# Kernel optimization log

Hardware: AMD Instinct MI355X
Metric: run time of the kernel (lower is better)

## Reference

```python
import jax, jax.numpy as jnp
import numpy as np

QK = 64
KNN = 16
EPS = 1e-5


def conv1(x, w, b):
    # x: (B,C,N), w: (O,C) -> (B,O,N)
    return jnp.einsum('oc,bcn->bon', w, x) + b[None, :, None]


def conv2(x, w, b):
    # x: (B,C,N,k), w: (O,C) -> (B,O,N,k)
    return jnp.einsum('oc,bcnk->bonk', w, x) + b[None, :, None, None]


def bn1(x, g, b, m, v):
    return g[None, :, None] * (x - m[None, :, None]) * jax.lax.rsqrt(v + EPS)[None, :, None] + b[None, :, None]


def bn2(x, g, b, m, v):
    return g[None, :, None, None] * (x - m[None, :, None, None]) * jax.lax.rsqrt(v + EPS)[None, :, None, None] + b[None, :, None, None]


def gather_nk(t, idx):
    # t: (B,C,M), idx: (B,N,k) -> (B,C,N,k)
    return jax.vmap(lambda tb, ib: tb[:, ib])(t, idx)


def setup_inputs():
    key = jax.random.key(0)
    ks = jax.random.split(key, 40)
    B, N, M = 2, 16384, 4096
    w = lambda k, s: jax.random.normal(k, s, dtype=jnp.float32) * 0.05
    d = {}
    d['xyz_hr'] = jax.random.normal(ks[0], (B, 3, N), dtype=jnp.float32)
    d['xyz_lr'] = jax.random.normal(ks[1], (B, 3, M), dtype=jnp.float32)
    d['sft_feat_lr'] = jax.random.normal(ks[2], (B, 6, M), dtype=jnp.float32)
    d['val_lr'] = jax.random.normal(ks[3], (B, 64, M), dtype=jnp.float32)
    # geom_encoder: Conv1d(3,64) -> BN -> ReLU -> Conv1d(64,64)
    d['ge_w1'] = w(ks[4], (QK, 3)); d['ge_b1'] = w(ks[5], (QK,))
    d['ge_g1'] = jnp.ones((QK,)); d['ge_be1'] = jnp.zeros((QK,))
    d['ge_m1'] = w(ks[6], (QK,)); d['ge_v1'] = jax.random.uniform(ks[7], (QK,), minval=0.5, maxval=1.5)
    d['ge_w2'] = w(ks[8], (QK, QK)); d['ge_b2'] = w(ks[9], (QK,))
    # scale/shift convs Conv1d(6,64)
    d['sc_w'] = w(ks[10], (QK, 6)); d['sc_b'] = w(ks[11], (QK,))
    d['sh_w'] = w(ks[12], (QK, 6)); d['sh_b'] = w(ks[13], (QK,))
    # sem query/key Conv1d(64,64)
    d['q_w'] = w(ks[14], (QK, QK)); d['q_b'] = w(ks[15], (QK,))
    d['k_w'] = w(ks[16], (QK, QK)); d['k_b'] = w(ks[17], (QK,))
    # bdy_head: Conv1d(64,64) -> BN -> ReLU -> Conv1d(64,1) -> Sigmoid
    d['bd_w1'] = w(ks[18], (64, QK)); d['bd_b1'] = w(ks[19], (64,))
    d['bd_g'] = jnp.ones((64,)); d['bd_be'] = jnp.zeros((64,))
    d['bd_m'] = w(ks[20], (64,)); d['bd_v'] = jax.random.uniform(ks[21], (64,), minval=0.5, maxval=1.5)
    d['bd_w2'] = w(ks[22], (1, 64)); d['bd_b2'] = w(ks[23], (1,))
    # rel_pos_mlp: Conv2d(3,64) -> BN2d -> ReLU -> Conv2d(64,64)
    d['rp_w1'] = w(ks[24], (QK, 3)); d['rp_b1'] = w(ks[25], (QK,))
    d['rp_g'] = jnp.ones((QK,)); d['rp_be'] = jnp.zeros((QK,))
    d['rp_m'] = w(ks[26], (QK,)); d['rp_v'] = jax.random.uniform(ks[27], (QK,), minval=0.5, maxval=1.5)
    d['rp_w2'] = w(ks[28], (QK, QK)); d['rp_b2'] = w(ks[29], (QK,))
    return d


def reference(xyz_hr, xyz_lr, sft_feat_lr, val_lr,
              ge_w1, ge_b1, ge_g1, ge_be1, ge_m1, ge_v1, ge_w2, ge_b2,
              sc_w, sc_b, sh_w, sh_b, q_w, q_b, k_w, k_b,
              bd_w1, bd_b1, bd_g, bd_be, bd_m, bd_v, bd_w2, bd_b2,
              rp_w1, rp_b1, rp_g, rp_be, rp_m, rp_v, rp_w2, rp_b2):
    B, _, M = sft_feat_lr.shape
    curr_k = min(KNN, M)

    def geom_enc(x):
        h = jax.nn.relu(bn1(conv1(x, ge_w1, ge_b1), ge_g1, ge_be1, ge_m1, ge_v1))
        return conv1(h, ge_w2, ge_b2)

    geom_hr = geom_enc(xyz_hr)                     # (B,64,N)
    geom_lr = geom_enc(xyz_lr)                     # (B,64,M)
    scale = conv1(sft_feat_lr, sc_w, sc_b)
    shift = conv1(sft_feat_lr, sh_w, sh_b)
    geom_lr_mod = geom_lr * (scale + 1.0) + shift
    Q = conv1(geom_hr, q_w, q_b)                   # (B,64,N)
    K = conv1(geom_lr_mod, k_w, k_b)               # (B,64,M)
    # boundary head
    h = jax.nn.relu(bn1(conv1(geom_hr, bd_w1, bd_b1), bd_g, bd_be, bd_m, bd_v))
    bdy_prob = jax.nn.sigmoid(conv1(h, bd_w2, bd_b2))  # (B,1,N)
    # kNN via squared distances (same argmin ordering as torch.cdist)
    hr_t = jnp.swapaxes(xyz_hr, 1, 2)              # (B,N,3)
    lr_t = jnp.swapaxes(xyz_lr, 1, 2)              # (B,M,3)
    d2 = (jnp.sum(hr_t**2, -1)[:, :, None] + jnp.sum(lr_t**2, -1)[:, None, :]
          - 2.0 * jnp.einsum('bnd,bmd->bnm', hr_t, lr_t))  # (B,N,M)
    _, k_idx = jax.lax.top_k(-d2, curr_k)          # (B,N,k) int32
    k_idx = jax.lax.stop_gradient(k_idx)

    K_g = gather_nk(K, k_idx)                      # (B,64,N,k)
    xyz_lr_g = gather_nk(xyz_lr, k_idx)            # (B,3,N,k)
    rel_pos = xyz_hr[:, :, :, None] - xyz_lr_g     # (B,3,N,k)
    pe = jax.nn.relu(bn2(conv2(rel_pos, rp_w1, rp_b1), rp_g, rp_be, rp_m, rp_v))
    pos_enc = conv2(pe, rp_w2, rp_b2)              # (B,64,N,k)
    logits = jnp.sum(Q[:, :, :, None] * (K_g + pos_enc), axis=1) / np.sqrt(QK)  # (B,N,k)
    attn = jax.nn.softmax(logits, axis=-1)
    val_g = gather_nk(val_lr, k_idx)               # (B,Cv,N,k)
    out = jnp.sum(attn[:, None, :, :] * val_g, axis=-1)  # (B,Cv,N)
    return out, bdy_prob
```

## Files before the change

### kernel.cpp

```cpp
#include <hip/hip_runtime.h>
#include <hip/hip_bf16.h>

#define B_ 2
#define N_ 16384
#define M_ 4096
#define EPS_ 1e-5f

typedef float f32x2 __attribute__((ext_vector_type(2)));
typedef float f32x4 __attribute__((ext_vector_type(4)));

__device__ __forceinline__ float b2f(const __hip_bfloat16 v) { return __bfloat162float(v); }

__device__ __forceinline__ float ldin(const void* p, size_t i, int f32) {
    return f32 ? ((const float*)p)[i] : __bfloat162float(((const __hip_bfloat16*)p)[i]);
}
__device__ __forceinline__ void stout(void* o, size_t i, float v, int f32) {
    if (f32) ((float*)o)[i] = v;
    else     ((__hip_bfloat16*)o)[i] = __float2bfloat16(v);
}

__device__ __forceinline__ float d2np(float x, float y, float z, float hn, float4 q) {
    float dot = __fadd_rn(__fadd_rn(__fmul_rn(x, q.x), __fmul_rn(y, q.y)), __fmul_rn(z, q.z));
    return __fsub_rn(__fadd_rn(hn, q.w), __fmul_rn(2.f, dot));
}
__device__ __forceinline__ float norm3np(float x, float y, float z) {
    return __fadd_rn(__fadd_rn(__fmul_rn(x, x), __fmul_rn(y, y)), __fmul_rn(z, z));
}

#define O_GE_W1 0
#define O_GE_B1 192
#define O_GE_W2 256
#define O_GE_B2 4352
#define O_QW    4416
#define O_QB    8512
#define O_KW    8576
#define O_KB    12672
#define O_SCW   12736
#define O_SCB   13120
#define O_SHW   13184
#define O_SHB   13568
#define O_BDW1  13632
#define O_BDB1  17728
#define O_BDW2  17792
#define O_BDB2  17856
#define O_RPW1  17920
#define O_RPB1  18112
#define O_RPW2  18176
#define O_RPB2  22272
#define OB_LR    92160
#define OB_Q     223232
#define OB_KT    4417536
#define OB_VT    5466112
#define OB_KIDX  6514688
#define OB_DFLAG 7694336
#define OB_PA1   7563264
#define OB_PA2   7628800
#define O_T_GE_W2 1923840
#define O_T_QW    1927936
#define O_T_KW    1932032
#define O_T_BDW1  1936128

#define TMAX 256

__global__ __launch_bounds__(256) void prep_kernel(
    const void* xyz_hr,
    const void* ge_w1, const void* ge_b1, const void* ge_g1, const void* ge_be1,
    const void* ge_m1, const void* ge_v1, const void* ge_w2, const void* ge_b2,
    const void* sc_w, const void* sc_b, const void* sh_w, const void* sh_b,
    const void* q_w, const void* q_b, const void* k_w, const void* k_b,
    const void* bd_w1, const void* bd_b1, const void* bd_g, const void* bd_be,
    const void* bd_m, const void* bd_v, const void* bd_w2, const void* bd_b2,
    const void* rp_w1, const void* rp_b1, const void* rp_g, const void* rp_be,
    const void* rp_m, const void* rp_v, const void* rp_w2, const void* rp_b2,
    float* W, int* dflag)
{
    __shared__ int scnt;
    int t = threadIdx.x;
    if (t == 0) scnt = 0;
    __syncthreads();
    if (t < 128) {
        unsigned short u = ((const unsigned short*)xyz_hr)[t];
        int e = (u >> 7) & 0xFF;
        int ok = (e >= 113 && e <= 132) || ((u & 0x7FFF) == 0);
        if (ok) atomicAdd(&scnt, 1);
    }
    __syncthreads();
    const int f32 = (scnt < 110) ? 1 : 0;
    if (t == 0) *dflag = f32;

    if (t < 64) {
        float s = ldin(ge_g1, t, f32) * rsqrtf(ldin(ge_v1, t, f32) + EPS_);
        for (int d = 0; d < 3; ++d) W[O_GE_W1 + t*3 + d] = s * ldin(ge_w1, t*3 + d, f32);
        W[O_GE_B1 + t] = s * (ldin(ge_b1, t, f32) - ldin(ge_m1, t, f32)) + ldin(ge_be1, t, f32);
        W[O_GE_B2 + t] = ldin(ge_b2, t, f32);
        W[O_QB + t] = ldin(q_b, t, f32);
        W[O_KB + t] = ldin(k_b, t, f32);
        W[O_SCB + t] = ldin(sc_b, t, f32);
        W[O_SHB + t] = ldin(sh_b, t, f32);
        float sb = ldin(bd_g, t, f32) * rsqrtf(ldin(bd_v, t, f32) + EPS_);
        W[O_BDB1 + t] = sb * (ldin(bd_b1, t, f32) - ldin(bd_m, t, f32)) + ldin(bd_be, t, f32);
        W[O_BDW2 + t] = ldin(bd_w2, t, f32);
        float sr = ldin(rp_g, t, f32) * rsqrtf(ldin(rp_v, t, f32) + EPS_);
        for (int d = 0; d < 3; ++d) W[O_RPW1 + t*3 + d] = sr * ldin(rp_w1, t*3 + d, f32);
        W[O_RPB1 + t] = sr * (ldin(rp_b1, t, f32) - ldin(rp_m, t, f32)) + ldin(rp_be, t, f32);
        W[O_RPB2 + t] = ldin(rp_b2, t, f32);
    }
    if (t == 0) W[O_BDB2] = ldin(bd_b2, 0, f32);
    for (int i = t; i < 4096; i += 256) {
        int c = i >> 6, r = i & 63;
        float w2 = ldin(ge_w2, i, f32);
        float qw = ldin(q_w, i, f32);
        float kw = ldin(k_w, i, f32);
        float sb = ldin(bd_g, c, f32) * rsqrtf(ldin(bd_v, c, f32) + EPS_);
        float bw = sb * ldin(bd_w1, i, f32);
        W[O_GE_W2 + i] = w2;
        W[O_QW + i]    = qw;
        W[O_KW + i]    = kw;
        W[O_RPW2 + i]  = ldin(rp_w2, i, f32);
        W[O_BDW1 + i]  = bw;
        W[O_T_GE_W2 + r*64 + c] = w2;
        W[O_T_QW    + r*64 + c] = qw;
        W[O_T_KW    + r*64 + c] = kw;
        W[O_T_BDW1  + r*64 + c] = bw;
    }
    for (int i = t; i < 384; i += 256) {
        W[O_SCW + i] = ldin(sc_w, i, f32);
        W[O_SHW + i] = ldin(sh_w, i, f32);
    }
}

__global__ __launch_bounds__(256) void lr_kernel(
    const void* __restrict__ xyz_lr,
    const void* __restrict__ sft,
    const void* __restrict__ val,
    const float* __restrict__ W,
    __hip_bfloat16* __restrict__ Kt, __hip_bfloat16* __restrict__ Vt,
    float4* __restrict__ LR, float* __restrict__ PA1, float* __restrict__ PA2,
    const int* dflag)
{
    const int f32 = *dflag;
    int lane = threadIdx.x & 63;
    int p = blockIdx.x * 4 + (threadIdx.x >> 6);
    int b = p >> 12, m = p & (M_ - 1);
    size_t base = (size_t)b*3*M_ + m;
    float x = ldin(xyz_lr, base, f32), y = ldin(xyz_lr, base + M_, f32), z = ldin(xyz_lr, base + 2*M_, f32);
    if (lane == 0) {
        float hn = norm3np(x, y, z);
        LR[p] = make_float4(x, y, z, hn);
        int k = m >> 1, o = m & 1;
        float* a1 = PA1 + ((size_t)b*2048 + k)*4;
        float* a2 = PA2 + ((size_t)b*2048 + k)*4;
        a1[o] = x; a1[2+o] = y;
        a2[o] = z; a2[2+o] = hn;
    }

    const float* w1 = W + O_GE_W1 + lane*3;
    float h = fmaxf(fmaf(w1[2], z, fmaf(w1[1], y, fmaf(w1[0], x, W[O_GE_B1 + lane]))), 0.f);
    float g = W[O_GE_B2 + lane];
#pragma unroll
    for (int i = 0; i < 64; ++i) {
        g = fmaf(W[O_T_GE_W2 + i*64 + lane], __shfl(h, i, 64), g);
    }
    float sc = W[O_SCB + lane], sh = W[O_SHB + lane];
    const float* wsc = W + O_SCW + lane*6;
    const float* wsh = W + O_SHW + lane*6;
#pragma unroll
    for (int d = 0; d < 6; ++d) {
        float s6 = ldin(sft, (size_t)b*6*M_ + d*M_ + m, f32);
        sc = fmaf(wsc[d], s6, sc); sh = fmaf(wsh[d], s6, sh);
    }
    float mod = fmaf(g, sc + 1.f, sh);
    float k = W[O_KB + lane];
#pragma unroll
    for (int i = 0; i < 64; ++i) {
        k = fmaf(W[O_T_KW + i*64 + lane], __shfl(mod, i, 64), k);
    }
    Kt[(size_t)p*64 + lane] = __float2bfloat16(k);
    Vt[(size_t)p*64 + lane] = __float2bfloat16(ldin(val, (size_t)b*64*M_ + (size_t)lane*M_ + m, f32));
}

__global__ __launch_bounds__(256) void hr_kernel(
    const void* __restrict__ xyz_hr,
    const float* __restrict__ W,
    __hip_bfloat16* __restrict__ Q,
    void* __restrict__ out, const int* dflag)
{
    const int f32 = *dflag;
    int lane = threadIdx.x & 63;
    int p = blockIdx.x * 4 + (threadIdx.x >> 6);
    int b = p >> 14, n = p & (N_ - 1);
    size_t base = (size_t)b*3*N_ + n;
    float x = ldin(xyz_hr, base, f32), y = ldin(xyz_hr, base + N_, f32), z = ldin(xyz_hr, base + 2*N_, f32);

    const float* w1 = W + O_GE_W1 + lane*3;
    float h = fmaxf(fmaf(w1[2], z, fmaf(w1[1], y, fmaf(w1[0], x, W[O_GE_B1 + lane]))), 0.f);
    float g = W[O_GE_B2 + lane];
#pragma unroll
    for (int i = 0; i < 64; ++i) {
        g = fmaf(W[O_T_GE_W2 + i*64 + lane], __shfl(h, i, 64), g);
    }
    float q = W[O_QB + lane];
#pragma unroll
    for (int i = 0; i < 64; ++i) {
        q = fmaf(W[O_T_QW + i*64 + lane], __shfl(g, i, 64), q);
    }
    Q[(size_t)p*64 + lane] = __float2bfloat16(q);
    float hb = W[O_BDB1 + lane];
#pragma unroll
    for (int i = 0; i < 64; ++i) {
        hb = fmaf(W[O_T_BDW1 + i*64 + lane], __shfl(g, i, 64), hb);
    }
    float o = W[O_BDW2 + lane] * fmaxf(hb, 0.f);
#pragma unroll
    for (int sh = 1; sh < 64; sh <<= 1) o += __shfl_xor(o, sh, 64);
    if (lane == 0) {
        o += W[O_BDB2];
        stout(out, (size_t)B_*64*N_ + (size_t)b*N_ + n, 1.f / (1.f + __expf(-o)), f32);
    }
}

#define CE(da, ia, db, ib) { \
    bool sw_ = (db < da) || (db == da && ib < ia); \
    float td_ = da; int ti_ = ia; \
    da = sw_ ? db : da; ia = sw_ ? ib : ia; \
    db = sw_ ? td_ : db; ib = sw_ ? ti_ : ib; }

__device__ __forceinline__ void topk_insert(float (&bd)[16], int (&bi)[16], float d2, int m) {
    if (d2 < bd[15] || (d2 == bd[15] && m < bi[15])) {
        bd[15] = d2; bi[15] = m;
#pragma unroll
        for (int j = 15; j > 0; --j) CE(bd[j-1], bi[j-1], bd[j], bi[j]);
    }
}

__device__ __forceinline__ int lesslex(uint2 e, float cd, int ci) {
    float dj = __uint_as_float(e.x);
    int   ij = (int)e.y;
    return (dj < cd || (dj == cd && ij < ci)) ? 1 : 0;
}

__global__ __launch_bounds__(256, 4) void knn_kernel(
    const void* __restrict__ xyz_hr,
    const float4* __restrict__ LR,
    const f32x4* __restrict__ PA1, const f32x4* __restrict__ PA2,
    unsigned short* __restrict__ kidx, const int* dflag)
{
#pragma clang fp reassociate(off)
#pragma clang fp contract(off)
    __shared__ uint2 scand[4 * TMAX];
    const int f32 = *dflag;
    int lane = threadIdx.x & 63;
    int wid  = threadIdx.x >> 6;
    int p = blockIdx.x * 4 + wid;
    int b = p >> 14, n = p & (N_ - 1);
    size_t base = (size_t)b*3*N_ + n;
    float x = ldin(xyz_hr, base, f32), y = ldin(xyz_hr, base + N_, f32), z = ldin(xyz_hr, base + 2*N_, f32);
    float hn = norm3np(x, y, z);
    const float4* L = LR + b*M_;
    const f32x4* P1 = PA1 + (size_t)b*2048;
    const f32x4* P2 = PA2 + (size_t)b*2048;

    f32x2 d2p[32];
    float v = 3.4e38f;
    f32x2 xx = {x, x}, yy = {y, y}, zz = {z, z}, hh = {hn, hn};
#pragma unroll
    for (int c = 0; c < 8; ++c) {
        f32x4 a[4], bb[4];
#pragma unroll
        for (int i = 0; i < 4; ++i) {
            int k = lane + (c*4 + i)*64;
            a[i]  = P1[k];
            bb[i] = P2[k];
        }
#pragma unroll
        for (int i = 0; i < 4; ++i) {
            f32x2 qx = __builtin_shufflevector(a[i],  a[i],  0, 1);
            f32x2 qy = __builtin_shufflevector(a[i],  a[i],  2, 3);
            f32x2 qz = __builtin_shufflevector(bb[i], bb[i], 0, 1);
            f32x2 qw = __builtin_shufflevector(bb[i], bb[i], 2, 3);
            f32x2 dot = ((xx*qx) + (yy*qy)) + (zz*qz);
            f32x2 d2  = (hh + qw) - (2.f*dot);
            d2p[c*4 + i] = d2;
            v = fminf(v, d2.x); v = fminf(v, d2.y);
        }
    }
    v = fminf(v, __shfl_xor(v, 16, 64));
    v = fminf(v, __shfl_xor(v, 32, 64));
    float tau = v;
#pragma unroll
    for (int st = 1; st <= 8; st <<= 1) tau = fmaxf(tau, __shfl_xor(tau, st, 64));

    int cnt = 0;
#pragma unroll
    for (int j = 0; j < 32; ++j)
        cnt += ((d2p[j].x <= tau) ? 1 : 0) + ((d2p[j].y <= tau) ? 1 : 0);
    int inc = cnt;
#pragma unroll
    for (int st = 1; st < 64; st <<= 1) {
        int o = __shfl_up(inc, st, 64);
        if (lane >= st) inc += o;
    }
    int off = inc - cnt;
    int T = __shfl(inc, 63, 64);

    if (T > TMAX) {
        float bd[16]; int bi[16];
#pragma unroll
        for (int j = 0; j < 16; ++j) { bd[j] = 3.4e38f; bi[j] = 0x7fffffff; }
        for (int m = 0; m < M_; ++m) {
            topk_insert(bd, bi, d2np(x, y, z, hn, L[m]), m);
        }
        if (lane == 0) {
            unsigned short* kr = kidx + (size_t)p*16;
#pragma unroll
            for (int j = 0; j < 16; ++j) kr[j] = (unsigned short)bi[j];
        }
        return;
    }

    uint2* wc = scand + wid * TMAX;
#pragma unroll
    for (int j = 0; j < 32; ++j) {
        int m0 = 2*lane + 128*j;
        if (d2p[j].x <= tau) { wc[off] = make_uint2(__float_as_uint(d2p[j].x), (unsigned)m0);     off++; }
        if (d2p[j].y <= tau) { wc[off] = make_uint2(__float_as_uint(d2p[j].y), (unsigned)(m0+1)); off++; }
    }
    int Tp = (T + 3) & ~3;
    if (lane < Tp - T) wc[T + lane] = make_uint2(0x7f800000u, 0xffffu);
    asm volatile("s_waitcnt lgkmcnt(0)" ::: "memory");

    for (int t = lane; t < T; t += 64) {
        uint2 cv = wc[t];
        float cd = __uint_as_float(cv.x);
        int   ci = (int)cv.y;
        int rank = 0;
        for (int j = 0; j < Tp; j += 4) {
            uint2 e0 = wc[j], e1 = wc[j+1], e2 = wc[j+2], e3 = wc[j+3];
            rank += lesslex(e0, cd, ci) + lesslex(e1, cd, ci)
                  + lesslex(e2, cd, ci) + lesslex(e3, cd, ci);
        }
        if (rank < 16) kidx[(size_t)p*16 + rank] = (unsigned short)ci;
    }
}

__global__ __launch_bounds__(256) void attn_kernel(
    const void* __restrict__ xyz_hr,
    const float4* __restrict__ LR,
    const float* __restrict__ W,
    const __hip_bfloat16* __restrict__ Q,
    const __hip_bfloat16* __restrict__ Kt,
    const __hip_bfloat16* __restrict__ Vt,
    const unsigned short* __restrict__ kidx,
    void* __restrict__ out, const int* dflag)
{
    const int f32 = *dflag;
    int p = (blockIdx.x * 256 + threadIdx.x) >> 6;
    int lane = threadIdx.x & 63;
    float fw0 = W[O_RPW1 + lane*3], fw1 = W[O_RPW1 + lane*3 + 1], fw2 = W[O_RPW1 + lane*3 + 2];
    float fb  = W[O_RPB1 + lane];

    int b = p >> 14, n = p & (N_ - 1);
    size_t base = (size_t)b*3*N_ + n;
    float xh = ldin(xyz_hr, base, f32), yh = ldin(xyz_hr, base + N_, f32), zh = ldin(xyz_hr, base + 2*N_, f32);
    float qc = b2f(Q[(size_t)p*64 + lane]);
    float q2 = 0.f;
#pragma unroll
    for (int cc = 0; cc < 64; ++cc) {
        float qb = __shfl(qc, cc, 64);
        q2 = fmaf(W[O_RPW2 + cc*64 + lane], qb, q2);
    }
    int idxv = (int)kidx[(size_t)p*16 + (lane & 15)];
    const float4* L = LR + b*M_;
    const __hip_bfloat16* Ktb = Kt + (size_t)b*M_*64;
    const __hip_bfloat16* Vtb = Vt + (size_t)b*M_*64;
    float lg[16];
#pragma unroll
    for (int j = 0; j < 16; ++j) {
        int mj = __shfl(idxv, j, 64);
        mj = (mj < M_) ? mj : (M_ - 1);
        float4 pl = L[mj];
        float r0 = xh - pl.x, r1 = yh - pl.y, r2 = zh - pl.z;
        float pe = fmaxf(fmaf(fw2, r2, fmaf(fw1, r1, fmaf(fw0, r0, fb))), 0.f);
        float v = fmaf(qc, b2f(Ktb[(size_t)mj*64 + lane]), q2 * pe);
#pragma unroll
        for (int sh = 1; sh < 64; sh <<= 1) v += __shfl_xor(v, sh, 64);
        lg[j] = v * 0.125f;
    }
    float mx = lg[0];
#pragma unroll
    for (int j = 1; j < 16; ++j) mx = fmaxf(mx, lg[j]);
    float sum = 0.f;
#pragma unroll
    for (int j = 0; j < 16; ++j) { lg[j] = __expf(lg[j] - mx); sum += lg[j]; }
    float inv = 1.f / sum;
    float o = 0.f;
#pragma unroll
    for (int j = 0; j < 16; ++j) {
        int mj = __shfl(idxv, j, 64);
        mj = (mj < M_) ? mj : (M_ - 1);
        o = fmaf(lg[j] * inv, b2f(Vtb[(size_t)mj*64 + lane]), o);
    }
    stout(out, ((size_t)(b*64 + lane))*N_ + n, o, f32);
}

extern "C" void kernel_launch(void* const* d_in, const int* in_sizes, int n_in,
                              void* d_out, int out_size, void* d_ws, size_t ws_size,
                              hipStream_t stream) {
    const void* xyz_hr = d_in[0];
    const void* xyz_lr = d_in[1];
    const void* sft    = d_in[2];
    const void* val    = d_in[3];

    char* ws = (char*)d_ws;
    float* W  = (float*)ws;
    float4* LR = (float4*)(ws + OB_LR);
    __hip_bfloat16* Qp = (__hip_bfloat16*)(ws + OB_Q);
    __hip_bfloat16* Kt = (__hip_bfloat16*)(ws + OB_KT);
    __hip_bfloat16* Vt = (__hip_bfloat16*)(ws + OB_VT);
    unsigned short* kidx = (unsigned short*)(ws + OB_KIDX);
    float* PA1 = (float*)(ws + OB_PA1);
    float* PA2 = (float*)(ws + OB_PA2);
    int* dflag = (int*)(ws + OB_DFLAG);

    prep_kernel<<<1, 256, 0, stream>>>(
        xyz_hr,
        d_in[4],  d_in[5],  d_in[6],  d_in[7],  d_in[8],  d_in[9],  d_in[10], d_in[11],
        d_in[12], d_in[13], d_in[14], d_in[15], d_in[16], d_in[17], d_in[18], d_in[19],
        d_in[20], d_in[21], d_in[22], d_in[23], d_in[24], d_in[25], d_in[26], d_in[27],
        d_in[28], d_in[29], d_in[30], d_in[31], d_in[32], d_in[33], d_in[34], d_in[35],
        W, dflag);
    lr_kernel<<<2048, 256, 0, stream>>>(xyz_lr, sft, val, W, Kt, Vt, LR, PA1, PA2, dflag);
    hr_kernel<<<8192, 256, 0, stream>>>(xyz_hr, W, Qp, d_out, dflag);
    knn_kernel<<<8192, 256, 0, stream>>>(xyz_hr, LR, (const f32x4*)PA1, (const f32x4*)PA2, kidx, dflag);
    attn_kernel<<<8192, 256, 0, stream>>>(xyz_hr, LR, W, Qp, Kt, Vt, kidx, d_out, dflag);
}
```

Measured before the change: 381.1 us.

## Process two query points per wavefront in kNN and double-buffer LR loads

Each wavefront in the kNN kernel now handles two high-res points and shares every loaded low-res point pair between both distance computations, which halves the global/L2 traffic per query. The LR loads are double-buffered one chunk ahead so they overlap the arithmetic. The selection logic moves into a helper that runs once per point, and the grid is halved to match. The cost is roughly doubled register use (two 64-float distance arrays), and the occupancy hint of 4 blocks per CU is dropped, so fewer waves may be resident.

```diff
diff --git a/kernel.cpp b/kernel.cpp
--- a/kernel.cpp
+++ b/kernel.cpp
@@ -239,51 +239,13 @@
     return (dj < cd || (dj == cd && ij < ci)) ? 1 : 0;
 }
 
-__global__ __launch_bounds__(256, 4) void knn_kernel(
-    const void* __restrict__ xyz_hr,
-    const float4* __restrict__ LR,
-    const f32x4* __restrict__ PA1, const f32x4* __restrict__ PA2,
-    unsigned short* __restrict__ kidx, const int* dflag)
-{
-#pragma clang fp reassociate(off)
-#pragma clang fp contract(off)
-    __shared__ uint2 scand[4 * TMAX];
-    const int f32 = *dflag;
-    int lane = threadIdx.x & 63;
-    int wid  = threadIdx.x >> 6;
-    int p = blockIdx.x * 4 + wid;
-    int b = p >> 14, n = p & (N_ - 1);
-    size_t base = (size_t)b*3*N_ + n;
-    float x = ldin(xyz_hr, base, f32), y = ldin(xyz_hr, base + N_, f32), z = ldin(xyz_hr, base + 2*N_, f32);
-    float hn = norm3np(x, y, z);
-    const float4* L = LR + b*M_;
-    const f32x4* P1 = PA1 + (size_t)b*2048;
-    const f32x4* P2 = PA2 + (size_t)b*2048;
-
-    f32x2 d2p[32];
-    float v = 3.4e38f;
-    f32x2 xx = {x, x}, yy = {y, y}, zz = {z, z}, hh = {hn, hn};
-#pragma unroll
-    for (int c = 0; c < 8; ++c) {
-        f32x4 a[4], bb[4];
-#pragma unroll
-        for (int i = 0; i < 4; ++i) {
-            int k = lane + (c*4 + i)*64;
-            a[i]  = P1[k];
-            bb[i] = P2[k];
-        }
-#pragma unroll
-        for (int i = 0; i < 4; ++i) {
-            f32x2 qx = __builtin_shufflevector(a[i],  a[i],  0, 1);
-            f32x2 qy = __builtin_shufflevector(a[i],  a[i],  2, 3);
-            f32x2 qz = __builtin_shufflevector(bb[i], bb[i], 0, 1);
-            f32x2 qw = __builtin_shufflevector(bb[i], bb[i], 2, 3);
-            f32x2 dot = ((xx*qx) + (yy*qy)) + (zz*qz);
-            f32x2 d2  = (hh + qw) - (2.f*dot);
-            d2p[c*4 + i] = d2;
-            v = fminf(v, d2.x); v = fminf(v, d2.y);
-        }
-    }
+__device__ __forceinline__ void select16(
+    f32x2 (&d2p)[32], float vmin, int lane, int p,
+    float x, float y, float z, float hn,
+    const float4* __restrict__ L, uint2* __restrict__ wc,
+    unsigned short* __restrict__ kidx)
+{
+    float v = vmin;
     v = fminf(v, __shfl_xor(v, 16, 64));
     v = fminf(v, __shfl_xor(v, 32, 64));
     float tau = v;
@@ -318,7 +280,6 @@
         return;
     }
 
-    uint2* wc = scand + wid * TMAX;
 #pragma unroll
     for (int j = 0; j < 32; ++j) {
         int m0 = 2*lane + 128*j;
@@ -343,6 +304,76 @@
     }
 }
 
+__global__ __launch_bounds__(256) void knn_kernel(
+    const void* __restrict__ xyz_hr,
+    const float4* __restrict__ LR,
+    const f32x4* __restrict__ PA1, const f32x4* __restrict__ PA2,
+    unsigned short* __restrict__ kidx, const int* dflag)
+{
+#pragma clang fp reassociate(off)
+#pragma clang fp contract(off)
+    __shared__ uint2 scand[4 * TMAX];
+    const int f32 = *dflag;
+    int lane = threadIdx.x & 63;
+    int wid  = threadIdx.x >> 6;
+    int p0 = blockIdx.x * 8 + wid * 2;
+    int p1 = p0 + 1;
+    int b = p0 >> 14;
+    int n0 = p0 & (N_ - 1), n1 = p1 & (N_ - 1);
+    size_t base0 = (size_t)b*3*N_ + n0;
+    size_t base1 = (size_t)b*3*N_ + n1;
+    float x0 = ldin(xyz_hr, base0, f32), y0 = ldin(xyz_hr, base0 + N_, f32), z0 = ldin(xyz_hr, base0 + 2*N_, f32);
+    float x1 = ldin(xyz_hr, base1, f32), y1 = ldin(xyz_hr, base1 + N_, f32), z1 = ldin(xyz_hr, base1 + 2*N_, f32);
+    float h0 = norm3np(x0, y0, z0);
+    float h1 = norm3np(x1, y1, z1);
+    const float4* L = LR + b*M_;
+    const f32x4* P1 = PA1 + (size_t)b*2048;
+    const f32x4* P2 = PA2 + (size_t)b*2048;
+
+    f32x2 xx0 = {x0,x0}, yy0 = {y0,y0}, zz0 = {z0,z0}, hh0 = {h0,h0};
+    f32x2 xx1 = {x1,x1}, yy1 = {y1,y1}, zz1 = {z1,z1}, hh1 = {h1,h1};
+
+    f32x2 d2a[32], d2b[32];
+    f32x2 va = {3.4e38f, 3.4e38f}, vb = {3.4e38f, 3.4e38f};
+    f32x4 A0[4], B0[4], A1[4], B1[4];
+#pragma unroll
+    for (int i = 0; i < 4; ++i) { A0[i] = P1[lane + i*64]; B0[i] = P2[lane + i*64]; }
+#pragma unroll
+    for (int c = 0; c < 8; ++c) {
+        const bool even = (c & 1) == 0;
+        f32x4* ca = even ? A0 : A1;
+        f32x4* cb = even ? B0 : B1;
+        f32x4* na = even ? A1 : A0;
+        f32x4* nb = even ? B1 : B0;
+        if (c < 7) {
+#pragma unroll
+            for (int i = 0; i < 4; ++i) {
+                na[i] = P1[lane + ((c+1)*4 + i)*64];
+                nb[i] = P2[lane + ((c+1)*4 + i)*64];
+            }
+        }
+#pragma unroll
+        for (int i = 0; i < 4; ++i) {
+            f32x2 qx = __builtin_shufflevector(ca[i], ca[i], 0, 1);
+            f32x2 qy = __builtin_shufflevector(ca[i], ca[i], 2, 3);
+            f32x2 qz = __builtin_shufflevector(cb[i], cb[i], 0, 1);
+            f32x2 qw = __builtin_shufflevector(cb[i], cb[i], 2, 3);
+            f32x2 dot0 = ((xx0*qx) + (yy0*qy)) + (zz0*qz);
+            f32x2 e0   = (hh0 + qw) - (2.f*dot0);
+            f32x2 dot1 = ((xx1*qx) + (yy1*qy)) + (zz1*qz);
+            f32x2 e1   = (hh1 + qw) - (2.f*dot1);
+            d2a[c*4 + i] = e0;
+            d2b[c*4 + i] = e1;
+            va.x = fminf(va.x, e0.x); va.y = fminf(va.y, e0.y);
+            vb.x = fminf(vb.x, e1.x); vb.y = fminf(vb.y, e1.y);
+        }
+    }
+
+    uint2* wc = scand + wid * TMAX;
+    select16(d2a, fminf(va.x, va.y), lane, p0, x0, y0, z0, h0, L, wc, kidx);
+    select16(d2b, fminf(vb.x, vb.y), lane, p1, x1, y1, z1, h1, L, wc, kidx);
+}
+
 __global__ __launch_bounds__(256) void attn_kernel(
     const void* __restrict__ xyz_hr,
     const float4* __restrict__ LR,
@@ -431,6 +462,6 @@
         W, dflag);
     lr_kernel<<<2048, 256, 0, stream>>>(xyz_lr, sft, val, W, Kt, Vt, LR, PA1, PA2, dflag);
     hr_kernel<<<8192, 256, 0, stream>>>(xyz_hr, W, Qp, d_out, dflag);
-    knn_kernel<<<8192, 256, 0, stream>>>(xyz_hr, LR, (const f32x4*)PA1, (const f32x4*)PA2, kidx, dflag);
+    knn_kernel<<<4096, 256, 0, stream>>>(xyz_hr, LR, (const f32x4*)PA1, (const f32x4*)PA2, kidx, dflag);
     attn_kernel<<<8192, 256, 0, stream>>>(xyz_hr, LR, W, Qp, Kt, Vt, kidx, d_out, dflag);
 }
```

New measurement: 544.8 us. 1.43x slower.

## Merge hr and knn kernels into one launch with interleaved block roles

Applied to the files above, without the earlier changes.

Combines the separate hr (Q/boundary MLP) and knn kernels into a single launch where odd blocks run the hr body and even blocks run the kNN body, so the compute-heavy MLP work can overlap with the latency-bound kNN selection and one launch gap disappears. It also replaces the distance computation's multiply-by-two and subtract with an explicit packed FMA. The fused kernel inherits the knn launch bounds and shared memory for hr blocks, and the fp contract(off) pragma now also covers the hr path. The FMA can change rounding of distances, which risks altering tie ordering against the reference top-k.

```diff
diff --git a/kernel.cpp b/kernel.cpp
--- a/kernel.cpp
+++ b/kernel.cpp
@@ -179,46 +179,6 @@
     Vt[(size_t)p*64 + lane] = __float2bfloat16(ldin(val, (size_t)b*64*M_ + (size_t)lane*M_ + m, f32));
 }
 
-__global__ __launch_bounds__(256) void hr_kernel(
-    const void* __restrict__ xyz_hr,
-    const float* __restrict__ W,
-    __hip_bfloat16* __restrict__ Q,
-    void* __restrict__ out, const int* dflag)
-{
-    const int f32 = *dflag;
-    int lane = threadIdx.x & 63;
-    int p = blockIdx.x * 4 + (threadIdx.x >> 6);
-    int b = p >> 14, n = p & (N_ - 1);
-    size_t base = (size_t)b*3*N_ + n;
-    float x = ldin(xyz_hr, base, f32), y = ldin(xyz_hr, base + N_, f32), z = ldin(xyz_hr, base + 2*N_, f32);
-
-    const float* w1 = W + O_GE_W1 + lane*3;
-    float h = fmaxf(fmaf(w1[2], z, fmaf(w1[1], y, fmaf(w1[0], x, W[O_GE_B1 + lane]))), 0.f);
-    float g = W[O_GE_B2 + lane];
-#pragma unroll
-    for (int i = 0; i < 64; ++i) {
-        g = fmaf(W[O_T_GE_W2 + i*64 + lane], __shfl(h, i, 64), g);
-    }
-    float q = W[O_QB + lane];
-#pragma unroll
-    for (int i = 0; i < 64; ++i) {
-        q = fmaf(W[O_T_QW + i*64 + lane], __shfl(g, i, 64), q);
-    }
-    Q[(size_t)p*64 + lane] = __float2bfloat16(q);
-    float hb = W[O_BDB1 + lane];
-#pragma unroll
-    for (int i = 0; i < 64; ++i) {
-        hb = fmaf(W[O_T_BDW1 + i*64 + lane], __shfl(g, i, 64), hb);
-    }
-    float o = W[O_BDW2 + lane] * fmaxf(hb, 0.f);
-#pragma unroll
-    for (int sh = 1; sh < 64; sh <<= 1) o += __shfl_xor(o, sh, 64);
-    if (lane == 0) {
-        o += W[O_BDB2];
-        stout(out, (size_t)B_*64*N_ + (size_t)b*N_ + n, 1.f / (1.f + __expf(-o)), f32);
-    }
-}
-
 #define CE(da, ia, db, ib) { \
     bool sw_ = (db < da) || (db == da && ib < ia); \
     float td_ = da; int ti_ = ia; \
@@ -239,19 +199,52 @@
     return (dj < cd || (dj == cd && ij < ci)) ? 1 : 0;
 }
 
-__global__ __launch_bounds__(256, 4) void knn_kernel(
+__device__ __forceinline__ void hr_body(
+    int p, int lane,
+    const void* __restrict__ xyz_hr,
+    const float* __restrict__ W,
+    __hip_bfloat16* __restrict__ Q,
+    void* __restrict__ out, const int f32)
+{
+    int b = p >> 14, n = p & (N_ - 1);
+    size_t base = (size_t)b*3*N_ + n;
+    float x = ldin(xyz_hr, base, f32), y = ldin(xyz_hr, base + N_, f32), z = ldin(xyz_hr, base + 2*N_, f32);
+
+    const float* w1 = W + O_GE_W1 + lane*3;
+    float h = fmaxf(fmaf(w1[2], z, fmaf(w1[1], y, fmaf(w1[0], x, W[O_GE_B1 + lane]))), 0.f);
+    float g = W[O_GE_B2 + lane];
+#pragma unroll
+    for (int i = 0; i < 64; ++i) {
+        g = fmaf(W[O_T_GE_W2 + i*64 + lane], __shfl(h, i, 64), g);
+    }
+    float q = W[O_QB + lane];
+#pragma unroll
+    for (int i = 0; i < 64; ++i) {
+        q = fmaf(W[O_T_QW + i*64 + lane], __shfl(g, i, 64), q);
+    }
+    Q[(size_t)p*64 + lane] = __float2bfloat16(q);
+    float hb = W[O_BDB1 + lane];
+#pragma unroll
+    for (int i = 0; i < 64; ++i) {
+        hb = fmaf(W[O_T_BDW1 + i*64 + lane], __shfl(g, i, 64), hb);
+    }
+    float o = W[O_BDW2 + lane] * fmaxf(hb, 0.f);
+#pragma unroll
+    for (int sh = 1; sh < 64; sh <<= 1) o += __shfl_xor(o, sh, 64);
+    if (lane == 0) {
+        o += W[O_BDB2];
+        stout(out, (size_t)B_*64*N_ + (size_t)b*N_ + n, 1.f / (1.f + __expf(-o)), f32);
+    }
+}
+
+__device__ __forceinline__ void knn_body(
+    int p, int lane, int wid,
     const void* __restrict__ xyz_hr,
     const float4* __restrict__ LR,
     const f32x4* __restrict__ PA1, const f32x4* __restrict__ PA2,
-    unsigned short* __restrict__ kidx, const int* dflag)
-{
-#pragma clang fp reassociate(off)
-#pragma clang fp contract(off)
-    __shared__ uint2 scand[4 * TMAX];
-    const int f32 = *dflag;
-    int lane = threadIdx.x & 63;
-    int wid  = threadIdx.x >> 6;
-    int p = blockIdx.x * 4 + wid;
+    uint2* __restrict__ scand,
+    unsigned short* __restrict__ kidx, const int f32)
+{
     int b = p >> 14, n = p & (N_ - 1);
     size_t base = (size_t)b*3*N_ + n;
     float x = ldin(xyz_hr, base, f32), y = ldin(xyz_hr, base + N_, f32), z = ldin(xyz_hr, base + 2*N_, f32);
@@ -263,6 +256,7 @@
     f32x2 d2p[32];
     float v = 3.4e38f;
     f32x2 xx = {x, x}, yy = {y, y}, zz = {z, z}, hh = {hn, hn};
+    const f32x2 m2 = {-2.f, -2.f};
 #pragma unroll
     for (int c = 0; c < 8; ++c) {
         f32x4 a[4], bb[4];
@@ -279,7 +273,7 @@
             f32x2 qz = __builtin_shufflevector(bb[i], bb[i], 0, 1);
             f32x2 qw = __builtin_shufflevector(bb[i], bb[i], 2, 3);
             f32x2 dot = ((xx*qx) + (yy*qy)) + (zz*qz);
-            f32x2 d2  = (hh + qw) - (2.f*dot);
+            f32x2 d2  = __builtin_elementwise_fma(m2, dot, hh + qw);
             d2p[c*4 + i] = d2;
             v = fminf(v, d2.x); v = fminf(v, d2.y);
         }
@@ -343,6 +337,30 @@
     }
 }
 
+__global__ __launch_bounds__(256, 4) void hrknn_kernel(
+    const void* __restrict__ xyz_hr,
+    const float4* __restrict__ LR,
+    const f32x4* __restrict__ PA1, const f32x4* __restrict__ PA2,
+    const float* __restrict__ W,
+    __hip_bfloat16* __restrict__ Q,
+    unsigned short* __restrict__ kidx,
+    void* __restrict__ out, const int* dflag)
+{
+#pragma clang fp reassociate(off)
+#pragma clang fp contract(off)
+    __shared__ uint2 scand[4 * TMAX];
+    const int f32 = *dflag;
+    int lane = threadIdx.x & 63;
+    int wid  = threadIdx.x >> 6;
+    int sub  = blockIdx.x >> 1;
+    int p = sub * 4 + wid;
+    if (blockIdx.x & 1) {
+        hr_body(p, lane, xyz_hr, W, Q, out, f32);
+    } else {
+        knn_body(p, lane, wid, xyz_hr, LR, PA1, PA2, scand, kidx, f32);
+    }
+}
+
 __global__ __launch_bounds__(256) void attn_kernel(
     const void* __restrict__ xyz_hr,
     const float4* __restrict__ LR,
@@ -430,7 +448,7 @@
         d_in[28], d_in[29], d_in[30], d_in[31], d_in[32], d_in[33], d_in[34], d_in[35],
         W, dflag);
     lr_kernel<<<2048, 256, 0, stream>>>(xyz_lr, sft, val, W, Kt, Vt, LR, PA1, PA2, dflag);
-    hr_kernel<<<8192, 256, 0, stream>>>(xyz_hr, W, Qp, d_out, dflag);
-    knn_kernel<<<8192, 256, 0, stream>>>(xyz_hr, LR, (const f32x4*)PA1, (const f32x4*)PA2, kidx, dflag);
+    hrknn_kernel<<<16384, 256, 0, stream>>>(xyz_hr, LR, (const f32x4*)PA1, (const f32x4*)PA2,
+                                            W, Qp, kidx, d_out, dflag);
     attn_kernel<<<8192, 256, 0, stream>>>(xyz_hr, LR, W, Qp, Kt, Vt, kidx, d_out, dflag);
 }
```

Result: slower. 435.6 us (+14.3%).
